# Optimization experiments

Measured on AMD Instinct MI355X. Metric: run time of the kernel, lower is better.

Reference implementation:

```python
import jax, jax.numpy as jnp
import numpy as np

ALPHA = 0.15
KSIZE = 5
EPS = 1e-6


def _minmax_norm(x):
    # x: [B,1,H,W]; per-sample min-max normalize, 0.5 if nearly constant
    mn = x.min(axis=(1, 2, 3), keepdims=True)
    mx = x.max(axis=(1, 2, 3), keepdims=True)
    denom = mx - mn
    safe = jnp.where(denom > EPS, denom, 1.0)
    return jnp.where(denom > EPS, (x - mn) / safe, 0.5)


def _saliency_map(images, out_hw):
    # grayscale via luma weights
    w = jnp.array([0.299, 0.587, 0.114], dtype=images.dtype).reshape(1, 3, 1, 1)
    gray = (images * w).sum(axis=1, keepdims=True)  # [B,1,H,W]
    kernel = jnp.ones((1, 1, KSIZE, KSIZE), dtype=gray.dtype) / (KSIZE * KSIZE)
    dn = ('NCHW', 'OIHW', 'NCHW')
    local_mean = jax.lax.conv_general_dilated(gray, kernel, (1, 1), 'SAME', dimension_numbers=dn)
    local_mean_sq = jax.lax.conv_general_dilated(gray ** 2, kernel, (1, 1), 'SAME', dimension_numbers=dn)
    local_var = jnp.maximum(local_mean_sq - local_mean ** 2, 0.0)
    sal = _minmax_norm(local_var)
    if sal.shape[-2:] != out_hw:
        sal = jax.image.resize(sal, (sal.shape[0], 1, out_hw[0], out_hw[1]), method='bilinear')
    return jax.lax.stop_gradient(sal)  # computed under no_grad / detached in torch


def setup_inputs() -> dict:
    key = jax.random.key(0)
    k1, k2 = jax.random.split(key)
    features = jax.random.normal(k1, (64, 512, 28, 28), dtype=jnp.float32)
    images = jax.random.uniform(k2, (64, 3, 224, 224), dtype=jnp.float32)
    return {"features": features, "images": images}


def reference(features, images):
    sal = _saliency_map(images, features.shape[-2:])  # [B,1,Hf,Wf]
    attn = jnp.sqrt((features ** 2).mean(axis=1, keepdims=True))  # [B,1,Hf,Wf]
    attn = _minmax_norm(attn)
    loss = jnp.mean((attn - sal) ** 2)
    return ALPHA * loss
```

## Files before the change

### kernel.cpp

```cpp
#include <hip/hip_runtime.h>
#include <math.h>

#define BATCH 64
#define HIMG 224
#define WIMG 224
#define IMGPLANE (HIMG*WIMG)
#define CF 512
#define HF 28
#define WF 28
#define POS (HF*WF)
#define ALPHA_C 0.15f
#define EPS_C 1e-6f

#define STRIPS 14
#define SROWS 16
#define GROWS 20
#define GSTR 229
#define VSTR 261
#define SHN 4580

#define NZ 16
#define CPG 32
#define NATTN 784
#define NVARH (STRIPS*BATCH)

#define OFF_HRES 0
#define HRES_CNT (BATCH*HIMG*WF)
#define OFF_BMM (OFF_HRES + HRES_CNT)
#define OFF_AP  (OFF_BMM + BATCH*STRIPS*2)
#define OFF_ACC (OFF_AP + NZ*BATCH*POS)
#define OFF_CNT (OFF_ACC + 1)

__global__ __launch_bounds__(256, 2) void fat_k(const float* __restrict__ img,
                                                const float* __restrict__ f,
                                                float* __restrict__ ws) {
    __shared__ float sh[SHN];
    __shared__ float wred[8];
    int bid = blockIdx.x;
    int tid = threadIdx.x;
    int g15 = bid / 15, r15 = bid - 15 * g15;

    if (r15 < 7) {
        int at = g15 * 7 + r15;
        if (at == 0 && tid == 0) {
            ws[OFF_ACC] = 0.0f;
            ((unsigned*)ws)[OFF_CNT] = 0u;
        }
        int t = at * 256 + tid;
        int b = t / (NZ * 196);
        int rem = t - b * (NZ * 196);
        int z = rem / 196, q = rem - z * 196;
        const float* fp = f + (size_t)(b * CF + z * CPG) * POS + 4 * q;
        float ax = 0.0f, ay = 0.0f, az = 0.0f, aw = 0.0f;
        #pragma unroll
        for (int c = 0; c < CPG; c++) {
            float4 u = *(const float4*)(fp + (size_t)c * POS);
            ax += u.x * u.x; ay += u.y * u.y;
            az += u.z * u.z; aw += u.w * u.w;
        }
        float4 o = make_float4(ax, ay, az, aw);
        *(float4*)(ws + OFF_AP + (size_t)(z * BATCH + b) * POS + 4 * q) = o;
        return;
    }

    int vb = g15 * 8 + (r15 - 7);
    int b = vb / STRIPS, sy = vb - b * STRIPS;
    int y0 = sy * SROWS;
    const float* imb = img + (size_t)b * 3 * IMGPLANE;

    for (int i = tid; i < GROWS * 56; i += 256) {
        int gr = i / 56, q = i - gr * 56;
        int gy = y0 - 2 + gr;
        float gx0 = 0.0f, gx1 = 0.0f, gx2 = 0.0f, gx3 = 0.0f;
        if ((unsigned)gy < HIMG) {
            const float* row = imb + gy * WIMG + 4 * q;
            float4 a = *(const float4*)(row);
            float4 bb = *(const float4*)(row + IMGPLANE);
            float4 c = *(const float4*)(row + 2 * IMGPLANE);
            gx0 = 0.299f * a.x + 0.587f * bb.x + 0.114f * c.x;
            gx1 = 0.299f * a.y + 0.587f * bb.y + 0.114f * c.y;
            gx2 = 0.299f * a.z + 0.587f * bb.z + 0.114f * c.z;
            gx3 = 0.299f * a.w + 0.587f * bb.w + 0.114f * c.w;
        }
        int base = gr * GSTR + 2 + 4 * q;
        sh[base] = gx0; sh[base + 1] = gx1; sh[base + 2] = gx2; sh[base + 3] = gx3;
    }
    if (tid < GROWS * 4) {
        int gr = tid >> 2, p = tid & 3;
        int gc = (p < 2) ? p : (224 + p);
        sh[gr * GSTR + gc] = 0.0f;
    }
    __syncthreads();

    int r = tid >> 4, s = tid & 15;
    int x0 = 14 * s;
    const float* gr0 = sh + r * GSTR;
    float c1[5], c2[5], vreg[14];
    #pragma unroll
    for (int m = 0; m < 5; m++) {
        float a = 0.0f, a2 = 0.0f;
        #pragma unroll
        for (int k = 0; k < 5; k++) {
            float u = gr0[k * GSTR + x0 + m];
            a += u; a2 += u * u;
        }
        c1[m] = a; c2[m] = a2;
    }
    float vmn = INFINITY, vmx = 0.0f;
    #pragma unroll
    for (int xi = 0; xi < 14; xi++) {
        int p = xi % 5;
        float s1 = c1[p], s2 = c2[p];
        #pragma unroll
        for (int m = 1; m < 5; m++) {
            s1 += c1[(p + m) % 5];
            s2 += c2[(p + m) % 5];
        }
        float m1 = s1 * 0.04f, m2 = s2 * 0.04f;
        float vv = fmaxf(m2 - m1 * m1, 0.0f);
        vreg[xi] = vv;
        vmn = fminf(vmn, vv); vmx = fmaxf(vmx, vv);
        if (xi < 13) {
            float a = 0.0f, a2 = 0.0f;
            #pragma unroll
            for (int k = 0; k < 5; k++) {
                float u = gr0[k * GSTR + x0 + xi + 5];
                a += u; a2 += u * u;
            }
            c1[p] = a; c2[p] = a2;
        }
    }
    #pragma unroll
    for (int o = 32; o > 0; o >>= 1) {
        vmn = fminf(vmn, __shfl_xor(vmn, o));
        vmx = fmaxf(vmx, __shfl_xor(vmx, o));
    }
    __syncthreads();
    int w = tid >> 6;
    if ((tid & 63) == 0) { wred[w] = vmn; wred[4 + w] = vmx; }
    if (tid < SROWS * 8) {
        int rr = tid >> 3, p = tid & 7;
        int jh = p + ((p < 4) ? 0 : 224);
        sh[rr * VSTR + jh + (jh >> 3)] = 0.0f;
    }
    #pragma unroll
    for (int xi = 0; xi < 14; xi++) {
        int jh = x0 + xi + 4;
        sh[r * VSTR + jh + (jh >> 3)] = vreg[xi];
    }
    __syncthreads();
    if (tid == 0) {
        float mn = fminf(fminf(wred[0], wred[1]), fminf(wred[2], wred[3]));
        float mx = fmaxf(fmaxf(wred[4], wred[5]), fmaxf(wred[6], wred[7]));
        int blk = b * STRIPS + sy;
        ws[OFF_BMM + 2 * blk]     = mn;
        ws[OFF_BMM + 2 * blk + 1] = mx;
    }

    float* hb = ws + OFF_HRES + ((size_t)b * HIMG + y0) * WF;
    for (int idx = tid; idx < SROWS * WF; idx += 256) {
        int rr = idx / WF, i = idx - rr * WF;
        float acc = 0.0f, wsum = 0.0f;
        int j0 = 8 * i - 4;
        #pragma unroll
        for (int t = 0; t < 16; t++) {
            int j = j0 + t;
            float w_ = 8.0f - fabsf((float)t - 7.5f);
            int jh = j + 4;
            acc += w_ * sh[rr * VSTR + jh + (jh >> 3)];
            if ((unsigned)j < WIMG) wsum += w_;
        }
        hb[idx] = acc / wsum;
    }
}

__global__ __launch_bounds__(256) void fused_k(float* __restrict__ ws,
                                               float* __restrict__ out) {
    __shared__ float hres[HIMG][WF + 1];
    __shared__ float wred[4];
    __shared__ float s_mn, s_mx;
    int b = blockIdx.x;
    int tid = threadIdx.x;

    if (tid < 64) {
        float mn = INFINITY, mx = 0.0f;
        if (tid < STRIPS) {
            mn = ws[OFF_BMM + 2 * (b * STRIPS + tid)];
            mx = ws[OFF_BMM + 2 * (b * STRIPS + tid) + 1];
        }
        #pragma unroll
        for (int o = 8; o > 0; o >>= 1) {
            mn = fminf(mn, __shfl_down(mn, o));
            mx = fmaxf(mx, __shfl_down(mx, o));
        }
        if (tid == 0) { s_mn = mn; s_mx = mx; }
    }

    const float* hg = ws + OFF_HRES + (size_t)b * HIMG * WF;
    for (int i = tid; i < HIMG * WF; i += 256) {
        int y = i / WF, x = i - y * WF;
        hres[y][x] = hg[i];
    }
    __syncthreads();

    float vmn = s_mn, vmx = s_mx;
    float vden = vmx - vmn;
    bool vok = vden > EPS_C;

    const float* ap = ws + OFF_AP + (size_t)b * POS;
    float salv[4], attnv[4];
    float amn = INFINITY, amx = -INFINITY;
    #pragma unroll
    for (int k = 0; k < 4; k++) {
        int idx = tid + 256 * k;
        salv[k] = 0.0f; attnv[k] = 0.0f;
        if (idx < POS) {
            int yo = idx / WF, x = idx - yo * WF;
            float acc = 0.0f, wsum = 0.0f;
            int j0 = 8 * yo - 4;
            #pragma unroll
            for (int t = 0; t < 16; t++) {
                int j = j0 + t;
                float w = 8.0f - fabsf((float)t - 7.5f);
                if ((unsigned)j < HIMG) { acc += w * hres[j][x]; wsum += w; }
            }
            float sraw = acc / wsum;
            salv[k] = vok ? (sraw - vmn) / vden : 0.5f;
            float ssum = 0.0f;
            #pragma unroll
            for (int z = 0; z < NZ; z++)
                ssum += ap[(size_t)z * BATCH * POS + idx];
            float a = sqrtf(ssum * (1.0f / CF));
            attnv[k] = a;
            amn = fminf(amn, a); amx = fmaxf(amx, a);
        }
    }

    #pragma unroll
    for (int o = 32; o > 0; o >>= 1) {
        amn = fminf(amn, __shfl_xor(amn, o));
        amx = fmaxf(amx, __shfl_xor(amx, o));
    }
    int w = tid >> 6;
    if ((tid & 63) == 0) wred[w] = amn;
    __syncthreads();
    if (tid == 0) s_mn = fminf(fminf(wred[0], wred[1]), fminf(wred[2], wred[3]));
    __syncthreads();
    if ((tid & 63) == 0) wred[w] = amx;
    __syncthreads();
    if (tid == 0) s_mx = fmaxf(fmaxf(wred[0], wred[1]), fmaxf(wred[2], wred[3]));
    __syncthreads();
    amn = s_mn; amx = s_mx;
    float aden = amx - amn;
    bool aok = aden > EPS_C;

    float lsum = 0.0f;
    #pragma unroll
    for (int k = 0; k < 4; k++) {
        int idx = tid + 256 * k;
        if (idx < POS) {
            float an = aok ? (attnv[k] - amn) / aden : 0.5f;
            float d = an - salv[k];
            lsum += d * d;
        }
    }
    #pragma unroll
    for (int o = 32; o > 0; o >>= 1) lsum += __shfl_xor(lsum, o);
    if ((tid & 63) == 0) wred[w] = lsum;
    __syncthreads();

    if (tid == 0) {
        float part = wred[0] + wred[1] + wred[2] + wred[3];
        atomicAdd(ws + OFF_ACC, part);
        __threadfence();
        unsigned old = atomicAdd((unsigned*)ws + OFF_CNT, 1u);
        if (old == BATCH - 1) {
            float tot = atomicAdd(ws + OFF_ACC, 0.0f);
            out[0] = tot * (ALPHA_C / (float)(BATCH * POS));
        }
    }
}

extern "C" void kernel_launch(void* const* d_in, const int* in_sizes, int n_in,
                              void* d_out, int out_size, void* d_ws, size_t ws_size,
                              hipStream_t stream) {
    const float* features = (const float*)d_in[0];
    const float* images   = (const float*)d_in[1];
    float* ws  = (float*)d_ws;
    float* out = (float*)d_out;

    hipLaunchKernelGGL(fat_k,   dim3(NATTN + NVARH), dim3(256), 0, stream,
                       images, features, ws);
    hipLaunchKernelGGL(fused_k, dim3(BATCH),         dim3(256), 0, stream, ws, out);
}
```

Baseline: 193.7 us.

## Split per-sample finalize across four blocks with last-block reduction; use nontemporal loads

The second kernel now runs four blocks per sample instead of one. Each block computes a quarter of the saliency and attention values, writes them to workspace, and publishes a partial min/max. A per-sample atomic counter picks the last block, which finishes the normalization and accumulates the loss. The shared-memory staging of the horizontal-resize buffer is dropped in favour of direct global reads. Streaming loads of features and images in the first kernel switch to nontemporal loads. The aim is to fill more compute units in the tail kernel, at the cost of extra global round-trips and atomics.

New measurement: 194.2 us. About the same (+0.3%).

```diff
diff --git a/kernel.cpp b/kernel.cpp
--- a/kernel.cpp
+++ b/kernel.cpp
@@ -26,10 +26,20 @@
 
 #define OFF_HRES 0
 #define HRES_CNT (BATCH*HIMG*WF)
-#define OFF_BMM (OFF_HRES + HRES_CNT)
-#define OFF_AP  (OFF_BMM + BATCH*STRIPS*2)
-#define OFF_ACC (OFF_AP + NZ*BATCH*POS)
-#define OFF_CNT (OFF_ACC + 1)
+#define OFF_BMM  (OFF_HRES + HRES_CNT)
+#define OFF_AP   (OFF_BMM + BATCH*STRIPS*2)
+#define OFF_SAL  (OFF_AP + NZ*BATCH*POS)
+#define OFF_ATT  (OFF_SAL + BATCH*POS)
+#define OFF_PMM  (OFF_ATT + BATCH*POS)
+#define OFF_ACC  (OFF_PMM + BATCH*8)
+#define OFF_CNT  (OFF_ACC + 1)
+#define OFF_QCNT (OFF_CNT + 1)
+
+typedef float f4v __attribute__((ext_vector_type(4)));
+
+__device__ __forceinline__ f4v nt4(const float* p) {
+    return __builtin_nontemporal_load((const f4v*)p);
+}
 
 __global__ __launch_bounds__(256, 2) void fat_k(const float* __restrict__ img,
                                                 const float* __restrict__ f,
@@ -42,9 +52,12 @@
 
     if (r15 < 7) {
         int at = g15 * 7 + r15;
-        if (at == 0 && tid == 0) {
-            ws[OFF_ACC] = 0.0f;
-            ((unsigned*)ws)[OFF_CNT] = 0u;
+        if (at == 0) {
+            if (tid == 0) {
+                ws[OFF_ACC] = 0.0f;
+                ((unsigned*)ws)[OFF_CNT] = 0u;
+            }
+            if (tid < BATCH) ((unsigned*)ws)[OFF_QCNT + tid] = 0u;
         }
         int t = at * 256 + tid;
         int b = t / (NZ * 196);
@@ -54,7 +67,7 @@
         float ax = 0.0f, ay = 0.0f, az = 0.0f, aw = 0.0f;
         #pragma unroll
         for (int c = 0; c < CPG; c++) {
-            float4 u = *(const float4*)(fp + (size_t)c * POS);
+            f4v u = nt4(fp + (size_t)c * POS);
             ax += u.x * u.x; ay += u.y * u.y;
             az += u.z * u.z; aw += u.w * u.w;
         }
@@ -74,9 +87,9 @@
         float gx0 = 0.0f, gx1 = 0.0f, gx2 = 0.0f, gx3 = 0.0f;
         if ((unsigned)gy < HIMG) {
             const float* row = imb + gy * WIMG + 4 * q;
-            float4 a = *(const float4*)(row);
-            float4 bb = *(const float4*)(row + IMGPLANE);
-            float4 c = *(const float4*)(row + 2 * IMGPLANE);
+            f4v a = nt4(row);
+            f4v bb = nt4(row + IMGPLANE);
+            f4v c = nt4(row + 2 * IMGPLANE);
             gx0 = 0.299f * a.x + 0.587f * bb.x + 0.114f * c.x;
             gx1 = 0.299f * a.y + 0.587f * bb.y + 0.114f * c.y;
             gx2 = 0.299f * a.z + 0.587f * bb.z + 0.114f * c.z;
@@ -176,10 +189,11 @@
 
 __global__ __launch_bounds__(256) void fused_k(float* __restrict__ ws,
                                                float* __restrict__ out) {
-    __shared__ float hres[HIMG][WF + 1];
-    __shared__ float wred[4];
-    __shared__ float s_mn, s_mx;
-    int b = blockIdx.x;
+    __shared__ float wred[8];
+    __shared__ float s_vmn, s_vmx;
+    __shared__ int s_last;
+    int bid = blockIdx.x;
+    int b = bid >> 2, qt = bid & 3;
     int tid = threadIdx.x;
 
     if (tid < 64) {
@@ -193,74 +207,72 @@
             mn = fminf(mn, __shfl_down(mn, o));
             mx = fmaxf(mx, __shfl_down(mx, o));
         }
-        if (tid == 0) { s_mn = mn; s_mx = mx; }
-    }
-
-    const float* hg = ws + OFF_HRES + (size_t)b * HIMG * WF;
-    for (int i = tid; i < HIMG * WF; i += 256) {
-        int y = i / WF, x = i - y * WF;
-        hres[y][x] = hg[i];
-    }
-    __syncthreads();
-
-    float vmn = s_mn, vmx = s_mx;
+        if (tid == 0) { s_vmn = mn; s_vmx = mx; }
+    }
+    __syncthreads();
+    float vmn = s_vmn, vmx = s_vmx;
     float vden = vmx - vmn;
     bool vok = vden > EPS_C;
 
-    const float* ap = ws + OFF_AP + (size_t)b * POS;
-    float salv[4], attnv[4];
     float amn = INFINITY, amx = -INFINITY;
-    #pragma unroll
-    for (int k = 0; k < 4; k++) {
-        int idx = tid + 256 * k;
-        salv[k] = 0.0f; attnv[k] = 0.0f;
-        if (idx < POS) {
-            int yo = idx / WF, x = idx - yo * WF;
-            float acc = 0.0f, wsum = 0.0f;
-            int j0 = 8 * yo - 4;
-            #pragma unroll
-            for (int t = 0; t < 16; t++) {
-                int j = j0 + t;
-                float w = 8.0f - fabsf((float)t - 7.5f);
-                if ((unsigned)j < HIMG) { acc += w * hres[j][x]; wsum += w; }
-            }
-            float sraw = acc / wsum;
-            salv[k] = vok ? (sraw - vmn) / vden : 0.5f;
-            float ssum = 0.0f;
-            #pragma unroll
-            for (int z = 0; z < NZ; z++)
-                ssum += ap[(size_t)z * BATCH * POS + idx];
-            float a = sqrtf(ssum * (1.0f / CF));
-            attnv[k] = a;
-            amn = fminf(amn, a); amx = fmaxf(amx, a);
-        }
-    }
-
+    if (tid < 196) {
+        int idx = qt * 196 + tid;
+        int yo = idx / WF, x = idx - yo * WF;
+        const float* hg = ws + OFF_HRES + (size_t)b * HIMG * WF;
+        float acc = 0.0f, wsum = 0.0f;
+        int j0 = 8 * yo - 4;
+        #pragma unroll
+        for (int t = 0; t < 16; t++) {
+            int j = j0 + t;
+            float w = 8.0f - fabsf((float)t - 7.5f);
+            if ((unsigned)j < HIMG) { acc += w * hg[j * WF + x]; wsum += w; }
+        }
+        float sraw = acc / wsum;
+        float salres = vok ? (sraw - vmn) / vden : 0.5f;
+        const float* ap = ws + OFF_AP + (size_t)b * POS;
+        float ssum = 0.0f;
+        #pragma unroll
+        for (int z = 0; z < NZ; z++)
+            ssum += ap[(size_t)z * BATCH * POS + idx];
+        float a = sqrtf(ssum * (1.0f / CF));
+        ws[OFF_SAL + b * POS + idx] = salres;
+        ws[OFF_ATT + b * POS + idx] = a;
+        amn = a; amx = a;
+    }
     #pragma unroll
     for (int o = 32; o > 0; o >>= 1) {
         amn = fminf(amn, __shfl_xor(amn, o));
         amx = fmaxf(amx, __shfl_xor(amx, o));
     }
     int w = tid >> 6;
-    if ((tid & 63) == 0) wred[w] = amn;
-    __syncthreads();
-    if (tid == 0) s_mn = fminf(fminf(wred[0], wred[1]), fminf(wred[2], wred[3]));
-    __syncthreads();
-    if ((tid & 63) == 0) wred[w] = amx;
-    __syncthreads();
-    if (tid == 0) s_mx = fmaxf(fmaxf(wred[0], wred[1]), fmaxf(wred[2], wred[3]));
-    __syncthreads();
-    amn = s_mn; amx = s_mx;
-    float aden = amx - amn;
+    if ((tid & 63) == 0) { wred[w] = amn; wred[4 + w] = amx; }
+    __syncthreads();
+    if (tid == 0) {
+        float mn = fminf(fminf(wred[0], wred[1]), fminf(wred[2], wred[3]));
+        float mx = fmaxf(fmaxf(wred[4], wred[5]), fmaxf(wred[6], wred[7]));
+        ws[OFF_PMM + 8 * b + 2 * qt]     = mn;
+        ws[OFF_PMM + 8 * b + 2 * qt + 1] = mx;
+        __threadfence();
+        unsigned old = atomicAdd((unsigned*)ws + OFF_QCNT + b, 1u);
+        s_last = (old == 3u) ? 1 : 0;
+    }
+    __syncthreads();
+    if (!s_last) return;
+    __threadfence();
+
+    float fmn = fminf(fminf(ws[OFF_PMM + 8 * b + 0], ws[OFF_PMM + 8 * b + 2]),
+                      fminf(ws[OFF_PMM + 8 * b + 4], ws[OFF_PMM + 8 * b + 6]));
+    float fmx = fmaxf(fmaxf(ws[OFF_PMM + 8 * b + 1], ws[OFF_PMM + 8 * b + 3]),
+                      fmaxf(ws[OFF_PMM + 8 * b + 5], ws[OFF_PMM + 8 * b + 7]));
+    float aden = fmx - fmn;
     bool aok = aden > EPS_C;
-
     float lsum = 0.0f;
     #pragma unroll
     for (int k = 0; k < 4; k++) {
         int idx = tid + 256 * k;
         if (idx < POS) {
-            float an = aok ? (attnv[k] - amn) / aden : 0.5f;
-            float d = an - salv[k];
+            float an = aok ? (ws[OFF_ATT + b * POS + idx] - fmn) / aden : 0.5f;
+            float d = an - ws[OFF_SAL + b * POS + idx];
             lsum += d * d;
         }
     }
@@ -268,7 +280,6 @@
     for (int o = 32; o > 0; o >>= 1) lsum += __shfl_xor(lsum, o);
     if ((tid & 63) == 0) wred[w] = lsum;
     __syncthreads();
-
     if (tid == 0) {
         float part = wred[0] + wred[1] + wred[2] + wred[3];
         atomicAdd(ws + OFF_ACC, part);
@@ -291,5 +302,5 @@
 
     hipLaunchKernelGGL(fat_k,   dim3(NATTN + NVARH), dim3(256), 0, stream,
                        images, features, ws);
-    hipLaunchKernelGGL(fused_k, dim3(BATCH),         dim3(256), 0, stream, ws, out);
+    hipLaunchKernelGGL(fused_k, dim3(4 * BATCH),     dim3(256), 0, stream, ws, out);
 }
```
